# Kernel tuning notes

Measured on AMD Instinct MI355X. Metric: run time of the kernel, lower is better.

## Reference

```python
import jax, jax.numpy as jnp
import numpy as np

ENC_HID = 512
DEC_HID = 1024
IN_DIM = ENC_HID * 2 + DEC_HID  # 2048


def setup_inputs() -> dict:
    key = jax.random.key(0)
    k1, k2, k3, k4 = jax.random.split(key, 4)
    B, S = 64, 2048
    enc_outputs = jax.random.normal(k1, (B, S, 2 * ENC_HID), dtype=jnp.float32)
    dec_hidden = jax.random.normal(k2, (B, DEC_HID), dtype=jnp.float32)
    # nn.Linear(IN_DIM, 1): weight [1, IN_DIM], bias [1]
    bound = 1.0 / np.sqrt(IN_DIM)
    attn_w = jax.random.uniform(k3, (1, IN_DIM), minval=-bound, maxval=bound, dtype=jnp.float32)
    attn_b = jax.random.uniform(k4, (1,), minval=-bound, maxval=bound, dtype=jnp.float32)
    return {"enc_outputs": enc_outputs, "dec_hidden": dec_hidden, "attn_w": attn_w, "attn_b": attn_b}


def reference(enc_outputs, dec_hidden, attn_w, attn_b):
    # Split the [1, 2*enc+dec] weight instead of materializing repeat+concat.
    w_enc = attn_w[0, : 2 * ENC_HID]   # [2E]
    w_dec = attn_w[0, 2 * ENC_HID :]   # [D]
    # energy[b,s] = enc_outputs[b,s,:] . w_enc + dec_hidden[b,:] . w_dec + b
    energy = (
        jnp.einsum("bse,e->bs", enc_outputs, w_enc)
        + (dec_hidden @ w_dec)[:, None]
        + attn_b[0]
    )
    attn_weights = jax.nn.softmax(energy, axis=1)          # [B, S]
    context = jnp.einsum("bs,bse->be", attn_weights, enc_outputs)  # [B, 2E]
    return context
```

## Files before the change

kernel.cpp:

```cpp
#include <hip/hip_runtime.h>
#include <math.h>


namespace {

constexpr int B_     = 64;
constexpr int S_     = 2048;
constexpr int E_     = 1024;
constexpr int KCH    = 32;
constexpr int CHUNK  = S_ / KCH;
constexpr int WAVES  = 4;
constexpr int THREADS = WAVES * 64;
constexpr int SPW    = CHUNK / WAVES;

__global__ __launch_bounds__(THREADS) void attn_partial(
    const float* __restrict__ enc,
    const float* __restrict__ w,
    float* __restrict__ wc,
    float* __restrict__ wm,
    float* __restrict__ wz)
{
  const int blk  = blockIdx.x;
  const int b    = blk / KCH;
  const int k    = blk % KCH;
  const int tid  = threadIdx.x;
  const int wave = tid >> 6;
  const int lane = tid & 63;

  float4 wf[4];
#pragma unroll
  for (int j = 0; j < 4; ++j)
    wf[j] = *reinterpret_cast<const float4*>(w + j * 256 + lane * 4);

  float m = -INFINITY, z = 0.f;
  float4 c[4];
#pragma unroll
  for (int j = 0; j < 4; ++j) c[j] = make_float4(0.f, 0.f, 0.f, 0.f);

  const float* base = enc + ((size_t)b * S_ + (size_t)k * CHUNK) * E_;

  for (int i = 0; i < SPW; ++i) {
    const float* row = base + (size_t)(i * WAVES + wave) * E_;
    float4 v[4];
#pragma unroll
    for (int j = 0; j < 4; ++j)
      v[j] = *reinterpret_cast<const float4*>(row + j * 256 + lane * 4);

    float dot = 0.f;
#pragma unroll
    for (int j = 0; j < 4; ++j)
      dot += v[j].x * wf[j].x + v[j].y * wf[j].y +
             v[j].z * wf[j].z + v[j].w * wf[j].w;
#pragma unroll
    for (int off = 32; off >= 1; off >>= 1)
      dot += __shfl_xor(dot, off, 64);

    if (dot > m) {
      const float sc_ = __expf(m - dot);
      z *= sc_;
#pragma unroll
      for (int j = 0; j < 4; ++j) {
        c[j].x *= sc_; c[j].y *= sc_; c[j].z *= sc_; c[j].w *= sc_;
      }
      m = dot;
    }
    const float p = __expf(dot - m);
    z += p;
#pragma unroll
    for (int j = 0; j < 4; ++j) {
      c[j].x += p * v[j].x; c[j].y += p * v[j].y;
      c[j].z += p * v[j].z; c[j].w += p * v[j].w;
    }
  }

  __shared__ float sC[WAVES][E_];
  __shared__ float sM[WAVES], sZ[WAVES];
#pragma unroll
  for (int j = 0; j < 4; ++j)
    *reinterpret_cast<float4*>(&sC[wave][j * 256 + lane * 4]) = c[j];
  if (lane == 0) { sM[wave] = m; sZ[wave] = z; }
  __syncthreads();

  float M = sM[0];
#pragma unroll
  for (int wv = 1; wv < WAVES; ++wv) M = fmaxf(M, sM[wv]);
  float coef[WAVES];
  float Z = 0.f;
#pragma unroll
  for (int wv = 0; wv < WAVES; ++wv) {
    coef[wv] = __expf(sM[wv] - M);
    Z += coef[wv] * sZ[wv];
  }

  const int d = tid * 4;
  float4 acc = make_float4(0.f, 0.f, 0.f, 0.f);
#pragma unroll
  for (int wv = 0; wv < WAVES; ++wv) {
    const float4 v = *reinterpret_cast<const float4*>(&sC[wv][d]);
    acc.x += coef[wv] * v.x; acc.y += coef[wv] * v.y;
    acc.z += coef[wv] * v.z; acc.w += coef[wv] * v.w;
  }
  *reinterpret_cast<float4*>(wc + (size_t)blk * E_ + d) = acc;
  if (tid == 0) { wm[blk] = M; wz[blk] = Z; }
}

__global__ __launch_bounds__(256) void attn_final(
    const float* __restrict__ wc, const float* __restrict__ wm,
    const float* __restrict__ wz, float* __restrict__ out)
{
  const int b   = blockIdx.x;
  const int tid = threadIdx.x;

  float M = -INFINITY;
#pragma unroll
  for (int k = 0; k < KCH; ++k) M = fmaxf(M, wm[b * KCH + k]);

  float coef[KCH];
  float Z = 0.f;
#pragma unroll
  for (int k = 0; k < KCH; ++k) {
    coef[k] = __expf(wm[b * KCH + k] - M);
    Z += coef[k] * wz[b * KCH + k];
  }
  const float inv = 1.f / Z;

  const int d = tid * 4;
  float4 acc = make_float4(0.f, 0.f, 0.f, 0.f);
#pragma unroll
  for (int k = 0; k < KCH; ++k) {
    const float4 v =
        *reinterpret_cast<const float4*>(wc + ((size_t)(b * KCH + k)) * E_ + d);
    acc.x += coef[k] * v.x; acc.y += coef[k] * v.y;
    acc.z += coef[k] * v.z; acc.w += coef[k] * v.w;
  }
  *reinterpret_cast<float4*>(out + (size_t)b * E_ + d) =
      make_float4(acc.x * inv, acc.y * inv, acc.z * inv, acc.w * inv);
}

}

extern "C" void kernel_launch(void* const* d_in, const int* in_sizes, int n_in,
                              void* d_out, int out_size, void* d_ws, size_t ws_size,
                              hipStream_t stream) {
  const float* enc    = (const float*)d_in[0];
  const float* attn_w = (const float*)d_in[2];

  float* wc = (float*)d_ws;
  float* wm = wc + (size_t)B_ * KCH * E_;
  float* wz = wm + (size_t)B_ * KCH;

  attn_partial<<<dim3(B_ * KCH), dim3(THREADS), 0, stream>>>(enc, attn_w, wc, wm, wz);
  attn_final<<<dim3(B_), dim3(256), 0, stream>>>(wc, wm, wz, (float*)d_out);
}
```

Measured before the change: 110.1 us.

## Double-buffer enc rows in registers with nontemporal loads, two rows per wave

Each wave now handles two sequence rows per iteration and prefetches the next pair into registers while computing the current pair's dots and online-softmax updates. Loads of the streamed encoder data use nontemporal hints to avoid polluting the cache. The final reduction kernel is split into four 64-thread blocks per batch to spread work across more CUs. Register pressure rises from holding four extra row buffers, which may reduce occupancy.

```diff
diff --git a/kernel.cpp b/kernel.cpp
--- a/kernel.cpp
+++ b/kernel.cpp
@@ -4,14 +4,21 @@
 
 namespace {
 
-constexpr int B_     = 64;
-constexpr int S_     = 2048;
-constexpr int E_     = 1024;
-constexpr int KCH    = 32;
-constexpr int CHUNK  = S_ / KCH;
-constexpr int WAVES  = 4;
+typedef float f4 __attribute__((ext_vector_type(4)));
+
+constexpr int B_      = 64;
+constexpr int S_      = 2048;
+constexpr int E_      = 1024;
+constexpr int KCH     = 32;
+constexpr int CHUNK   = S_ / KCH;
+constexpr int WAVES   = 4;
 constexpr int THREADS = WAVES * 64;
-constexpr int SPW    = CHUNK / WAVES;
+constexpr int ROWS    = 2;
+constexpr int ITERS   = CHUNK / (WAVES * ROWS);
+
+__device__ __forceinline__ float dot4(const f4 a, const f4 b) {
+  return a.x * b.x + a.y * b.y + a.z * b.z + a.w * b.w;
+}
 
 __global__ __launch_bounds__(THREADS) void attn_partial(
     const float* __restrict__ enc,
@@ -27,65 +34,101 @@
   const int wave = tid >> 6;
   const int lane = tid & 63;
 
-  float4 wf[4];
+  f4 wf[4];
 #pragma unroll
   for (int j = 0; j < 4; ++j)
-    wf[j] = *reinterpret_cast<const float4*>(w + j * 256 + lane * 4);
+    wf[j] = *reinterpret_cast<const f4*>(w + j * 256 + lane * 4);
+
+  const float* base = enc + ((size_t)b * S_ + (size_t)k * CHUNK) * E_;
+  auto rowp = [&](int i, int rr) {
+    return base + (size_t)(i * (WAVES * ROWS) + wave * ROWS + rr) * E_ +
+           lane * 4;
+  };
+
+  f4 v0[4], v1[4], n0[4], n1[4];
+#pragma unroll
+  for (int j = 0; j < 4; ++j) {
+    v0[j] = __builtin_nontemporal_load(
+        reinterpret_cast<const f4*>(rowp(0, 0) + j * 256));
+    v1[j] = __builtin_nontemporal_load(
+        reinterpret_cast<const f4*>(rowp(0, 1) + j * 256));
+  }
 
   float m = -INFINITY, z = 0.f;
-  float4 c[4];
+  f4 c[4];
 #pragma unroll
-  for (int j = 0; j < 4; ++j) c[j] = make_float4(0.f, 0.f, 0.f, 0.f);
+  for (int j = 0; j < 4; ++j) c[j] = (f4)0.f;
 
-  const float* base = enc + ((size_t)b * S_ + (size_t)k * CHUNK) * E_;
+#pragma unroll 1
+  for (int i = 0; i < ITERS - 1; ++i) {
+#pragma unroll
+    for (int j = 0; j < 4; ++j) {
+      n0[j] = __builtin_nontemporal_load(
+          reinterpret_cast<const f4*>(rowp(i + 1, 0) + j * 256));
+      n1[j] = __builtin_nontemporal_load(
+          reinterpret_cast<const f4*>(rowp(i + 1, 1) + j * 256));
+    }
 
-  for (int i = 0; i < SPW; ++i) {
-    const float* row = base + (size_t)(i * WAVES + wave) * E_;
-    float4 v[4];
+    float d0 = 0.f, d1 = 0.f;
 #pragma unroll
-    for (int j = 0; j < 4; ++j)
-      v[j] = *reinterpret_cast<const float4*>(row + j * 256 + lane * 4);
+    for (int j = 0; j < 4; ++j) { d0 += dot4(v0[j], wf[j]); d1 += dot4(v1[j], wf[j]); }
+#pragma unroll
+    for (int off = 32; off >= 1; off >>= 1) {
+      d0 += __shfl_xor(d0, off, 64);
+      d1 += __shfl_xor(d1, off, 64);
+    }
 
-    float dot = 0.f;
-#pragma unroll
-    for (int j = 0; j < 4; ++j)
-      dot += v[j].x * wf[j].x + v[j].y * wf[j].y +
-             v[j].z * wf[j].z + v[j].w * wf[j].w;
-#pragma unroll
-    for (int off = 32; off >= 1; off >>= 1)
-      dot += __shfl_xor(dot, off, 64);
-
-    if (dot > m) {
-      const float sc_ = __expf(m - dot);
+    const float mx = fmaxf(d0, d1);
+    if (mx > m) {
+      const float sc_ = __expf(m - mx);
       z *= sc_;
 #pragma unroll
-      for (int j = 0; j < 4; ++j) {
-        c[j].x *= sc_; c[j].y *= sc_; c[j].z *= sc_; c[j].w *= sc_;
-      }
-      m = dot;
+      for (int j = 0; j < 4; ++j) c[j] *= sc_;
+      m = mx;
     }
-    const float p = __expf(dot - m);
-    z += p;
+    const float p0 = __expf(d0 - m), p1 = __expf(d1 - m);
+    z += p0 + p1;
 #pragma unroll
-    for (int j = 0; j < 4; ++j) {
-      c[j].x += p * v[j].x; c[j].y += p * v[j].y;
-      c[j].z += p * v[j].z; c[j].w += p * v[j].w;
+    for (int j = 0; j < 4; ++j) c[j] += p0 * v0[j] + p1 * v1[j];
+#pragma unroll
+    for (int j = 0; j < 4; ++j) { v0[j] = n0[j]; v1[j] = n1[j]; }
+  }
+  {
+    float d0 = 0.f, d1 = 0.f;
+#pragma unroll
+    for (int j = 0; j < 4; ++j) { d0 += dot4(v0[j], wf[j]); d1 += dot4(v1[j], wf[j]); }
+#pragma unroll
+    for (int off = 32; off >= 1; off >>= 1) {
+      d0 += __shfl_xor(d0, off, 64);
+      d1 += __shfl_xor(d1, off, 64);
     }
+    const float mx = fmaxf(d0, d1);
+    if (mx > m) {
+      const float sc_ = __expf(m - mx);
+      z *= sc_;
+#pragma unroll
+      for (int j = 0; j < 4; ++j) c[j] *= sc_;
+      m = mx;
+    }
+    const float p0 = __expf(d0 - m), p1 = __expf(d1 - m);
+    z += p0 + p1;
+#pragma unroll
+    for (int j = 0; j < 4; ++j) c[j] += p0 * v0[j] + p1 * v1[j];
   }
 
   __shared__ float sC[WAVES][E_];
   __shared__ float sM[WAVES], sZ[WAVES];
 #pragma unroll
   for (int j = 0; j < 4; ++j)
-    *reinterpret_cast<float4*>(&sC[wave][j * 256 + lane * 4]) = c[j];
+    *reinterpret_cast<f4*>(&sC[wave][j * 256 + lane * 4]) = c[j];
   if (lane == 0) { sM[wave] = m; sZ[wave] = z; }
   __syncthreads();
 
   float M = sM[0];
 #pragma unroll
   for (int wv = 1; wv < WAVES; ++wv) M = fmaxf(M, sM[wv]);
+  float Z = 0.f;
   float coef[WAVES];
-  float Z = 0.f;
 #pragma unroll
   for (int wv = 0; wv < WAVES; ++wv) {
     coef[wv] = __expf(sM[wv] - M);
@@ -93,23 +136,22 @@
   }
 
   const int d = tid * 4;
-  float4 acc = make_float4(0.f, 0.f, 0.f, 0.f);
+  f4 acc = (f4)0.f;
 #pragma unroll
-  for (int wv = 0; wv < WAVES; ++wv) {
-    const float4 v = *reinterpret_cast<const float4*>(&sC[wv][d]);
-    acc.x += coef[wv] * v.x; acc.y += coef[wv] * v.y;
-    acc.z += coef[wv] * v.z; acc.w += coef[wv] * v.w;
-  }
-  *reinterpret_cast<float4*>(wc + (size_t)blk * E_ + d) = acc;
+  for (int wv = 0; wv < WAVES; ++wv)
+    acc += coef[wv] * *reinterpret_cast<const f4*>(&sC[wv][d]);
+  *reinterpret_cast<f4*>(wc + (size_t)blk * E_ + d) = acc;
   if (tid == 0) { wm[blk] = M; wz[blk] = Z; }
 }
 
-__global__ __launch_bounds__(256) void attn_final(
+__global__ __launch_bounds__(64) void attn_final(
     const float* __restrict__ wc, const float* __restrict__ wm,
     const float* __restrict__ wz, float* __restrict__ out)
 {
-  const int b   = blockIdx.x;
-  const int tid = threadIdx.x;
+  const int blk  = blockIdx.x;
+  const int b    = blk >> 2;
+  const int q    = blk & 3;
+  const int lane = threadIdx.x;
 
   float M = -INFINITY;
 #pragma unroll
@@ -124,17 +166,14 @@
   }
   const float inv = 1.f / Z;
 
-  const int d = tid * 4;
-  float4 acc = make_float4(0.f, 0.f, 0.f, 0.f);
+  const int d = q * 256 + lane * 4;
+  f4 acc = (f4)0.f;
 #pragma unroll
-  for (int k = 0; k < KCH; ++k) {
-    const float4 v =
-        *reinterpret_cast<const float4*>(wc + ((size_t)(b * KCH + k)) * E_ + d);
-    acc.x += coef[k] * v.x; acc.y += coef[k] * v.y;
-    acc.z += coef[k] * v.z; acc.w += coef[k] * v.w;
-  }
-  *reinterpret_cast<float4*>(out + (size_t)b * E_ + d) =
-      make_float4(acc.x * inv, acc.y * inv, acc.z * inv, acc.w * inv);
+  for (int k = 0; k < KCH; ++k)
+    acc += coef[k] *
+           *reinterpret_cast<const f4*>(wc + ((size_t)(b * KCH + k)) * E_ + d);
+  acc *= inv;
+  *reinterpret_cast<f4*>(out + (size_t)b * E_ + d) = acc;
 }
 
 }
@@ -150,5 +189,5 @@
   float* wz = wm + (size_t)B_ * KCH;
 
   attn_partial<<<dim3(B_ * KCH), dim3(THREADS), 0, stream>>>(enc, attn_w, wc, wm, wz);
-  attn_final<<<dim3(B_), dim3(256), 0, stream>>>(wc, wm, wz, (float*)d_out);
+  attn_final<<<dim3(B_ * 4), dim3(64), 0, stream>>>(wc, wm, wz, (float*)d_out);
 }
```

New measurement: 94.91 us. -13.8%, faster.
